# Kernel optimization log

Hardware: AMD Instinct MI355X
Metric: run time of the kernel (lower is better)

Reference implementation:

```python
import jax, jax.numpy as jnp
import numpy as np

B, S, D = 64, 8192, 64

def setup_inputs() -> dict:
    key = jax.random.key(0)
    kq, kk, kv = jax.random.split(key, 3)
    q = jax.random.normal(kq, (B, S, D), dtype=jnp.float32)
    k = jax.random.normal(kk, (B, S, D), dtype=jnp.float32)
    v = jax.random.normal(kv, (B, S, D), dtype=jnp.float32)
    return {"q": q, "k": k, "v": v}

def _feature_map(x):
    # ELU(x) + 1
    return jax.nn.elu(x) + 1.0

def reference(q, k, v):
    qf = _feature_map(q)              # [B, S, D]
    kf = _feature_map(k)              # [B, S, D]
    k_sum = kf.sum(axis=-2)           # [B, D]
    kv = jnp.einsum('bsd,bse->bde', kf, v)        # [B, D, D]
    deno = jnp.maximum(jnp.einsum('bsd,bd->bs', qf, k_sum), 1e-4)  # [B, S]
    o = jnp.einsum('bsd,bde->bse', qf, kv) / deno[..., None]       # [B, S, D]
    return o
```

## Files before the change

### kernel.cpp

```cpp
#include <hip/hip_runtime.h>
#include <math.h>

#define BB 64
#define SS 8192
#define DD 64

constexpr int C1 = 8;
constexpr int CHUNK1 = SS / C1;
constexpr int TILES1 = CHUNK1 / 64;

typedef __attribute__((ext_vector_type(8))) short bf16x8;
typedef __attribute__((ext_vector_type(4))) float f32x4;

__device__ __forceinline__ float fmap(float x) {
    return x > 0.0f ? x + 1.0f : __expf(x);
}

__device__ __forceinline__ short f2bf(float x) {
    unsigned int u = __float_as_uint(x);
    u += 0x7FFFu + ((u >> 16) & 1u);
    return (short)(u >> 16);
}

__global__ __launch_bounds__(256) void phase1_kernel(
    const float* __restrict__ k,
    const float* __restrict__ v,
    float* __restrict__ kvT_ws,
    float* __restrict__ ksum_ws)
{
    __shared__ float Ks[2][64 * 64];
    __shared__ float Vs[2][64 * 64];

    const int t    = threadIdx.x;
    const int lane = t & 63;
    const int w    = t >> 6;
    const int b    = blockIdx.y;
    const int schunk = blockIdx.x * CHUNK1;

    const float* kb = k + (size_t)b * SS * DD;
    const float* vb = v + (size_t)b * SS * DD;

    const int d0  = (lane >> 3) * 8;
    const int e0  = (lane & 7) * 8;
    const int sw0 = w * 16;

    float acc[8][8] = {};
    float ksa[8] = {};

    {
        const float* kt = kb + (size_t)schunk * DD;
        const float* vt = vb + (size_t)schunk * DD;
        #pragma unroll
        for (int i = 0; i < 4; ++i) {
            const int idx = (t + i * 256) * 4;
            float4 kk = *(const float4*)(kt + idx);
            float4 vv = *(const float4*)(vt + idx);
            kk.x = fmap(kk.x); kk.y = fmap(kk.y);
            kk.z = fmap(kk.z); kk.w = fmap(kk.w);
            *(float4*)(&Ks[0][idx]) = kk;
            *(float4*)(&Vs[0][idx]) = vv;
        }
    }
    __syncthreads();

    for (int tile = 0; tile < TILES1; ++tile) {
        const int cur = tile & 1;
        float4 kreg[4], vreg[4];
        const bool pf = (tile < TILES1 - 1);
        if (pf) {
            const float* kt = kb + (size_t)(schunk + (tile + 1) * 64) * DD;
            const float* vt = vb + (size_t)(schunk + (tile + 1) * 64) * DD;
            #pragma unroll
            for (int i = 0; i < 4; ++i) {
                const int idx = (t + i * 256) * 4;
                kreg[i] = *(const float4*)(kt + idx);
                vreg[i] = *(const float4*)(vt + idx);
            }
        }
        const float* Kc = Ks[cur];
        const float* Vc = Vs[cur];
        #pragma unroll 4
        for (int s = 0; s < 16; ++s) {
            const float* krow = Kc + (sw0 + s) * 64;
            const float* vrow = Vc + (sw0 + s) * 64;
            float4 k0 = *(const float4*)(krow + d0);
            float4 k1 = *(const float4*)(krow + d0 + 4);
            float4 v0 = *(const float4*)(vrow + e0);
            float4 v1 = *(const float4*)(vrow + e0 + 4);
            const float kf[8] = {k0.x,k0.y,k0.z,k0.w,k1.x,k1.y,k1.z,k1.w};
            const float vv[8] = {v0.x,v0.y,v0.z,v0.w,v1.x,v1.y,v1.z,v1.w};
            #pragma unroll
            for (int i = 0; i < 8; ++i) {
                ksa[i] += kf[i];
                #pragma unroll
                for (int j = 0; j < 8; ++j) acc[i][j] += kf[i] * vv[j];
            }
        }
        if (pf) {
            float* Kn = Ks[cur ^ 1];
            float* Vn = Vs[cur ^ 1];
            #pragma unroll
            for (int i = 0; i < 4; ++i) {
                const int idx = (t + i * 256) * 4;
                float4 kk = kreg[i];
                kk.x = fmap(kk.x); kk.y = fmap(kk.y);
                kk.z = fmap(kk.z); kk.w = fmap(kk.w);
                *(float4*)(&Kn[idx]) = kk;
                *(float4*)(&Vn[idx]) = vreg[i];
            }
        }
        __syncthreads();
    }

    if ((lane & 7) == 0) {
        #pragma unroll
        for (int i = 0; i < 8; ++i)
            atomicAdd(ksum_ws + b * DD + d0 + i, ksa[i]);
    }

    float* scr0 = &Ks[0][0];
    float* scr1 = &Vs[0][0];
    if (w & 1) {
        float* dst = (w == 1) ? scr0 : scr1;
        #pragma unroll
        for (int i = 0; i < 8; ++i)
            #pragma unroll
            for (int jj = 0; jj < 2; ++jj)
                *(float4*)(dst + (i * 2 + jj) * 256 + lane * 4) =
                    make_float4(acc[i][jj*4], acc[i][jj*4+1], acc[i][jj*4+2], acc[i][jj*4+3]);
    }
    __syncthreads();
    if (!(w & 1)) {
        const float* src = (w == 0) ? scr0 : scr1;
        #pragma unroll
        for (int i = 0; i < 8; ++i)
            #pragma unroll
            for (int jj = 0; jj < 2; ++jj) {
                float4 x = *(const float4*)(src + (i * 2 + jj) * 256 + lane * 4);
                acc[i][jj*4]   += x.x;
                acc[i][jj*4+1] += x.y;
                acc[i][jj*4+2] += x.z;
                acc[i][jj*4+3] += x.w;
            }
    }
    __syncthreads();
    if (w == 2) {
        #pragma unroll
        for (int i = 0; i < 8; ++i)
            #pragma unroll
            for (int jj = 0; jj < 2; ++jj)
                *(float4*)(scr0 + (i * 2 + jj) * 256 + lane * 4) =
                    make_float4(acc[i][jj*4], acc[i][jj*4+1], acc[i][jj*4+2], acc[i][jj*4+3]);
    }
    __syncthreads();
    if (w == 0) {
        #pragma unroll
        for (int i = 0; i < 8; ++i)
            #pragma unroll
            for (int jj = 0; jj < 2; ++jj) {
                float4 x = *(const float4*)(scr0 + (i * 2 + jj) * 256 + lane * 4);
                acc[i][jj*4]   += x.x;
                acc[i][jj*4+1] += x.y;
                acc[i][jj*4+2] += x.z;
                acc[i][jj*4+3] += x.w;
            }
        float* kvb = kvT_ws + (size_t)b * DD * DD;
        #pragma unroll
        for (int i = 0; i < 8; ++i)
            #pragma unroll
            for (int j = 0; j < 8; ++j)
                atomicAdd(kvb + (e0 + j) * DD + (d0 + i), acc[i][j]);
    }
}

__global__ __launch_bounds__(256) void phase2_kernel(
    const float* __restrict__ q,
    const float* __restrict__ kvT_ws,
    const float* __restrict__ ksum_ws,
    float* __restrict__ o)
{
    const int t    = threadIdx.x;
    const int lane = t & 63;
    const int w    = t >> 6;
    const int b    = blockIdx.y;
    const int wid  = blockIdx.x * 4 + w;
    const int g    = lane >> 4;
    const int c    = lane & 15;

    const float* kvb = kvT_ws + (size_t)b * DD * DD;
    bf16x8 Bfrag[4][2];
    #pragma unroll
    for (int et = 0; et < 4; ++et) {
        #pragma unroll
        for (int dk = 0; dk < 2; ++dk) {
            const float* p = kvb + (et * 16 + c) * DD + dk * 32 + g * 8;
            float4 lo = *(const float4*)p;
            float4 hi = *(const float4*)(p + 4);
            bf16x8 f;
            f[0] = f2bf(lo.x); f[1] = f2bf(lo.y); f[2] = f2bf(lo.z); f[3] = f2bf(lo.w);
            f[4] = f2bf(hi.x); f[5] = f2bf(hi.y); f[6] = f2bf(hi.z); f[7] = f2bf(hi.w);
            Bfrag[et][dk] = f;
        }
    }
    float ksr[16];
    #pragma unroll
    for (int dk = 0; dk < 2; ++dk) {
        const float* p = ksum_ws + b * DD + dk * 32 + g * 8;
        float4 lo = *(const float4*)p;
        float4 hi = *(const float4*)(p + 4);
        ksr[dk*8+0] = lo.x; ksr[dk*8+1] = lo.y; ksr[dk*8+2] = lo.z; ksr[dk*8+3] = lo.w;
        ksr[dk*8+4] = hi.x; ksr[dk*8+5] = hi.y; ksr[dk*8+6] = hi.z; ksr[dk*8+7] = hi.w;
    }

    const float* qb = q + (size_t)b * SS * DD;
    float*       ob = o + (size_t)b * SS * DD;

    #pragma unroll 1
    for (int tt = 0; tt < 8; ++tt) {
        const int s0 = wid * 128 + tt * 16;
        const float* qrow = qb + (size_t)(s0 + c) * DD;
        float qf[16];
        #pragma unroll
        for (int dk = 0; dk < 2; ++dk) {
            float4 lo = *(const float4*)(qrow + dk * 32 + g * 8);
            float4 hi = *(const float4*)(qrow + dk * 32 + g * 8 + 4);
            qf[dk*8+0] = fmap(lo.x); qf[dk*8+1] = fmap(lo.y);
            qf[dk*8+2] = fmap(lo.z); qf[dk*8+3] = fmap(lo.w);
            qf[dk*8+4] = fmap(hi.x); qf[dk*8+5] = fmap(hi.y);
            qf[dk*8+6] = fmap(hi.z); qf[dk*8+7] = fmap(hi.w);
        }
        float dn = 0.0f;
        #pragma unroll
        for (int i = 0; i < 16; ++i) dn += qf[i] * ksr[i];
        dn += __shfl_xor(dn, 16, 64);
        dn += __shfl_xor(dn, 32, 64);

        bf16x8 A0, A1;
        #pragma unroll
        for (int i = 0; i < 8; ++i) { A0[i] = f2bf(qf[i]); A1[i] = f2bf(qf[8+i]); }

        f32x4 acc0 = {0.f,0.f,0.f,0.f}, acc1 = {0.f,0.f,0.f,0.f};
        f32x4 acc2 = {0.f,0.f,0.f,0.f}, acc3 = {0.f,0.f,0.f,0.f};
        acc0 = __builtin_amdgcn_mfma_f32_16x16x32_bf16(A0, Bfrag[0][0], acc0, 0, 0, 0);
        acc0 = __builtin_amdgcn_mfma_f32_16x16x32_bf16(A1, Bfrag[0][1], acc0, 0, 0, 0);
        acc1 = __builtin_amdgcn_mfma_f32_16x16x32_bf16(A0, Bfrag[1][0], acc1, 0, 0, 0);
        acc1 = __builtin_amdgcn_mfma_f32_16x16x32_bf16(A1, Bfrag[1][1], acc1, 0, 0, 0);
        acc2 = __builtin_amdgcn_mfma_f32_16x16x32_bf16(A0, Bfrag[2][0], acc2, 0, 0, 0);
        acc2 = __builtin_amdgcn_mfma_f32_16x16x32_bf16(A1, Bfrag[2][1], acc2, 0, 0, 0);
        acc3 = __builtin_amdgcn_mfma_f32_16x16x32_bf16(A0, Bfrag[3][0], acc3, 0, 0, 0);
        acc3 = __builtin_amdgcn_mfma_f32_16x16x32_bf16(A1, Bfrag[3][1], acc3, 0, 0, 0);

        #pragma unroll
        for (int r = 0; r < 4; ++r) {
            float dr  = __shfl(dn, (g << 2) + r, 64);
            float inv = 1.0f / fmaxf(dr, 1e-4f);
            float* op = ob + (size_t)(s0 + (g << 2) + r) * DD + c;
            op[0]  = acc0[r] * inv;
            op[16] = acc1[r] * inv;
            op[32] = acc2[r] * inv;
            op[48] = acc3[r] * inv;
        }
    }
}

extern "C" void kernel_launch(void* const* d_in, const int* in_sizes, int n_in,
                              void* d_out, int out_size, void* d_ws, size_t ws_size,
                              hipStream_t stream) {
    const float* q = (const float*)d_in[0];
    const float* k = (const float*)d_in[1];
    const float* v = (const float*)d_in[2];
    float* o = (float*)d_out;

    float* kvT_ws  = (float*)d_ws;
    float* ksum_ws = kvT_ws + (size_t)BB * DD * DD;
    const size_t ws_bytes = ((size_t)BB * DD * DD + (size_t)BB * DD) * sizeof(float);

    hipMemsetAsync(d_ws, 0, ws_bytes, stream);

    dim3 g1(C1, BB), g2(16, BB), blk(256);
    phase1_kernel<<<g1, blk, 0, stream>>>(k, v, kvT_ws, ksum_ws);
    phase2_kernel<<<g2, blk, 0, stream>>>(q, kvT_ws, ksum_ws, o);
}
```

Before: 463.3 us.

## Move phase1 KV accumulation to bf16x3 MFMA with async global-to-LDS loads

Rewrites the phase1 K^T·V reduction to use bf16 MFMA 16x16x32, keeping fp32-level accuracy by splitting each operand into hi/lo bf16 parts and issuing three MFMAs per tile. Tile loads now go through global_load_lds directly into swizzled LDS with 128-row tiles and double buffering, and the feature map is applied on LDS read instead of at staging. The final cross-wave reduction goes through LDS scratch with coalesced atomics. Phase1 is memory bound, so the gain depends on whether the faster load path and lower ALU pressure outweigh the extra split work and the LDS bank patterns.

```diff
diff --git a/kernel.cpp b/kernel.cpp
--- a/kernel.cpp
+++ b/kernel.cpp
@@ -7,7 +7,8 @@
 
 constexpr int C1 = 8;
 constexpr int CHUNK1 = SS / C1;
-constexpr int TILES1 = CHUNK1 / 64;
+constexpr int TROWS  = 128;
+constexpr int TILES1 = CHUNK1 / TROWS;
 
 typedef __attribute__((ext_vector_type(8))) short bf16x8;
 typedef __attribute__((ext_vector_type(4))) float f32x4;
@@ -20,6 +21,23 @@
     unsigned int u = __float_as_uint(x);
     u += 0x7FFFu + ((u >> 16) & 1u);
     return (short)(u >> 16);
+}
+
+__device__ __forceinline__ void split8(const float* x, bf16x8& hi, bf16x8& lo) {
+    #pragma unroll
+    for (int i = 0; i < 8; ++i) {
+        unsigned int u = __float_as_uint(x[i]);
+        hi[i] = (short)(u >> 16);
+        float l = x[i] - __uint_as_float(u & 0xFFFF0000u);
+        lo[i] = f2bf(l);
+    }
+}
+
+__device__ __forceinline__ void gload_lds16(const float* gsrc, float* ldst) {
+    __builtin_amdgcn_global_load_lds(
+        (const __attribute__((address_space(1))) unsigned int*)gsrc,
+        (__attribute__((address_space(3))) unsigned int*)ldst,
+        16, 0, 0);
 }
 
 __global__ __launch_bounds__(256) void phase1_kernel(
@@ -28,148 +46,113 @@
     float* __restrict__ kvT_ws,
     float* __restrict__ ksum_ws)
 {
-    __shared__ float Ks[2][64 * 64];
-    __shared__ float Vs[2][64 * 64];
+    __shared__ float Ks[2][TROWS * 64];
+    __shared__ float Vs[2][TROWS * 64];
 
     const int t    = threadIdx.x;
     const int lane = t & 63;
     const int w    = t >> 6;
+    const int g    = lane >> 4;
+    const int c    = lane & 15;
     const int b    = blockIdx.y;
-    const int schunk = blockIdx.x * CHUNK1;
-
-    const float* kb = k + (size_t)b * SS * DD;
-    const float* vb = v + (size_t)b * SS * DD;
-
-    const int d0  = (lane >> 3) * 8;
-    const int e0  = (lane & 7) * 8;
-    const int sw0 = w * 16;
-
-    float acc[8][8] = {};
-    float ksa[8] = {};
-
-    {
-        const float* kt = kb + (size_t)schunk * DD;
-        const float* vt = vb + (size_t)schunk * DD;
-        #pragma unroll
-        for (int i = 0; i < 4; ++i) {
-            const int idx = (t + i * 256) * 4;
-            float4 kk = *(const float4*)(kt + idx);
-            float4 vv = *(const float4*)(vt + idx);
-            kk.x = fmap(kk.x); kk.y = fmap(kk.y);
-            kk.z = fmap(kk.z); kk.w = fmap(kk.w);
-            *(float4*)(&Ks[0][idx]) = kk;
-            *(float4*)(&Vs[0][idx]) = vv;
-        }
-    }
+
+    const size_t base = (size_t)b * SS * DD + (size_t)blockIdx.x * CHUNK1 * DD;
+    const float* kb = k + base;
+    const float* vb = v + base;
+
+    auto issue_tile = [&](int tt, int buf) {
+        const float* kt = kb + tt * (TROWS * 64);
+        const float* vt = vb + tt * (TROWS * 64);
+        #pragma unroll
+        for (int i = 0; i < 8; ++i) {
+            const int Lidx = (w * 8 + i) * 64 + lane;
+            const int s    = Lidx >> 4;
+            const int p    = Lidx & 15;
+            const int gch  = p ^ (((s >> 3) & 1) << 2);
+            const int goff = s * 64 + gch * 4;
+            const int loff = (w * 8 + i) * 256;
+            gload_lds16(kt + goff, &Ks[buf][loff]);
+            gload_lds16(vt + goff, &Vs[buf][loff]);
+        }
+    };
+
+    f32x4 acc[4][4] = {};
+    float ksa[4] = {};
+
+    issue_tile(0, 0);
     __syncthreads();
 
-    for (int tile = 0; tile < TILES1; ++tile) {
-        const int cur = tile & 1;
-        float4 kreg[4], vreg[4];
-        const bool pf = (tile < TILES1 - 1);
-        if (pf) {
-            const float* kt = kb + (size_t)(schunk + (tile + 1) * 64) * DD;
-            const float* vt = vb + (size_t)(schunk + (tile + 1) * 64) * DD;
-            #pragma unroll
-            for (int i = 0; i < 4; ++i) {
-                const int idx = (t + i * 256) * 4;
-                kreg[i] = *(const float4*)(kt + idx);
-                vreg[i] = *(const float4*)(vt + idx);
-            }
-        }
+    for (int tt = 0; tt < TILES1; ++tt) {
+        const int cur = tt & 1;
+        if (tt + 1 < TILES1) issue_tile(tt + 1, cur ^ 1);
+
         const float* Kc = Ks[cur];
         const float* Vc = Vs[cur];
-        #pragma unroll 4
-        for (int s = 0; s < 16; ++s) {
-            const float* krow = Kc + (sw0 + s) * 64;
-            const float* vrow = Vc + (sw0 + s) * 64;
-            float4 k0 = *(const float4*)(krow + d0);
-            float4 k1 = *(const float4*)(krow + d0 + 4);
-            float4 v0 = *(const float4*)(vrow + e0);
-            float4 v1 = *(const float4*)(vrow + e0 + 4);
-            const float kf[8] = {k0.x,k0.y,k0.z,k0.w,k1.x,k1.y,k1.z,k1.w};
-            const float vv[8] = {v0.x,v0.y,v0.z,v0.w,v1.x,v1.y,v1.z,v1.w};
-            #pragma unroll
-            for (int i = 0; i < 8; ++i) {
-                ksa[i] += kf[i];
-                #pragma unroll
-                for (int j = 0; j < 8; ++j) acc[i][j] += kf[i] * vv[j];
+        const int srow = w * 32 + g * 8;
+        const int sw   = (g & 1) << 2;
+
+        bf16x8 Ah[4], Al[4];
+        #pragma unroll
+        for (int et = 0; et < 4; ++et) {
+            const int dc   = et * 16 + c;
+            const int bidx = srow * 64 + ((((dc >> 2) ^ sw)) << 2) + (dc & 3);
+            float x[8];
+            #pragma unroll
+            for (int i = 0; i < 8; ++i) x[i] = Vc[bidx + i * 64];
+            split8(x, Ah[et], Al[et]);
+        }
+        #pragma unroll
+        for (int dt = 0; dt < 4; ++dt) {
+            const int dc   = dt * 16 + c;
+            const int bidx = srow * 64 + ((((dc >> 2) ^ sw)) << 2) + (dc & 3);
+            float y[8];
+            #pragma unroll
+            for (int i = 0; i < 8; ++i) y[i] = fmap(Kc[bidx + i * 64]);
+            ksa[dt] += ((y[0] + y[1]) + (y[2] + y[3])) + ((y[4] + y[5]) + (y[6] + y[7]));
+            bf16x8 Bh, Bl;
+            split8(y, Bh, Bl);
+            #pragma unroll
+            for (int et = 0; et < 4; ++et) {
+                acc[et][dt] = __builtin_amdgcn_mfma_f32_16x16x32_bf16(Ah[et], Bh, acc[et][dt], 0, 0, 0);
+                acc[et][dt] = __builtin_amdgcn_mfma_f32_16x16x32_bf16(Ah[et], Bl, acc[et][dt], 0, 0, 0);
+                acc[et][dt] = __builtin_amdgcn_mfma_f32_16x16x32_bf16(Al[et], Bh, acc[et][dt], 0, 0, 0);
             }
         }
-        if (pf) {
-            float* Kn = Ks[cur ^ 1];
-            float* Vn = Vs[cur ^ 1];
-            #pragma unroll
-            for (int i = 0; i < 4; ++i) {
-                const int idx = (t + i * 256) * 4;
-                float4 kk = kreg[i];
-                kk.x = fmap(kk.x); kk.y = fmap(kk.y);
-                kk.z = fmap(kk.z); kk.w = fmap(kk.w);
-                *(float4*)(&Kn[idx]) = kk;
-                *(float4*)(&Vn[idx]) = vreg[i];
+        __syncthreads();
+    }
+
+    #pragma unroll
+    for (int dt = 0; dt < 4; ++dt) {
+        float s = ksa[dt];
+        s += __shfl_xor(s, 16, 64);
+        s += __shfl_xor(s, 32, 64);
+        ksa[dt] = s;
+    }
+    if (lane < 16) {
+        #pragma unroll
+        for (int dt = 0; dt < 4; ++dt)
+            atomicAdd(ksum_ws + b * DD + dt * 16 + lane, ksa[dt]);
+    }
+
+    float* scr = &Ks[0][0] + w * 4096;
+    #pragma unroll
+    for (int et = 0; et < 4; ++et)
+        #pragma unroll
+        for (int dt = 0; dt < 4; ++dt)
+            #pragma unroll
+            for (int r = 0; r < 4; ++r) {
+                const int e = et * 16 + 4 * g + r;
+                const int d = dt * 16 + c;
+                scr[e * 64 + d] = acc[et][dt][r];
             }
-        }
-        __syncthreads();
-    }
-
-    if ((lane & 7) == 0) {
-        #pragma unroll
-        for (int i = 0; i < 8; ++i)
-            atomicAdd(ksum_ws + b * DD + d0 + i, ksa[i]);
-    }
-
-    float* scr0 = &Ks[0][0];
-    float* scr1 = &Vs[0][0];
-    if (w & 1) {
-        float* dst = (w == 1) ? scr0 : scr1;
-        #pragma unroll
-        for (int i = 0; i < 8; ++i)
-            #pragma unroll
-            for (int jj = 0; jj < 2; ++jj)
-                *(float4*)(dst + (i * 2 + jj) * 256 + lane * 4) =
-                    make_float4(acc[i][jj*4], acc[i][jj*4+1], acc[i][jj*4+2], acc[i][jj*4+3]);
-    }
     __syncthreads();
-    if (!(w & 1)) {
-        const float* src = (w == 0) ? scr0 : scr1;
-        #pragma unroll
-        for (int i = 0; i < 8; ++i)
-            #pragma unroll
-            for (int jj = 0; jj < 2; ++jj) {
-                float4 x = *(const float4*)(src + (i * 2 + jj) * 256 + lane * 4);
-                acc[i][jj*4]   += x.x;
-                acc[i][jj*4+1] += x.y;
-                acc[i][jj*4+2] += x.z;
-                acc[i][jj*4+3] += x.w;
-            }
-    }
-    __syncthreads();
-    if (w == 2) {
-        #pragma unroll
-        for (int i = 0; i < 8; ++i)
-            #pragma unroll
-            for (int jj = 0; jj < 2; ++jj)
-                *(float4*)(scr0 + (i * 2 + jj) * 256 + lane * 4) =
-                    make_float4(acc[i][jj*4], acc[i][jj*4+1], acc[i][jj*4+2], acc[i][jj*4+3]);
-    }
-    __syncthreads();
-    if (w == 0) {
-        #pragma unroll
-        for (int i = 0; i < 8; ++i)
-            #pragma unroll
-            for (int jj = 0; jj < 2; ++jj) {
-                float4 x = *(const float4*)(scr0 + (i * 2 + jj) * 256 + lane * 4);
-                acc[i][jj*4]   += x.x;
-                acc[i][jj*4+1] += x.y;
-                acc[i][jj*4+2] += x.z;
-                acc[i][jj*4+3] += x.w;
-            }
-        float* kvb = kvT_ws + (size_t)b * DD * DD;
-        #pragma unroll
-        for (int i = 0; i < 8; ++i)
-            #pragma unroll
-            for (int j = 0; j < 8; ++j)
-                atomicAdd(kvb + (e0 + j) * DD + (d0 + i), acc[i][j]);
+    float* kvb = kvT_ws + (size_t)b * DD * DD;
+    const float* s0 = &Ks[0][0];
+    #pragma unroll
+    for (int jj = 0; jj < 16; ++jj) {
+        const int i = jj * 256 + t;
+        const float vsum = (s0[i] + s0[4096 + i]) + (s0[8192 + i] + s0[12288 + i]);
+        atomicAdd(kvb + i, vsum);
     }
 }
 
```

After: 416.3 us. 10.1% less time.
